# Optimization experiments

Measured on AMD Instinct MI355X. Metric: run time of the kernel, lower is better.

## Reference

```python
import jax, jax.numpy as jnp
import numpy as np

EPS_NORM = 1e-12
BN_EPS = 1e-5
TEMP = 0.07


def _l2norm(x, axis):
    n = jnp.sqrt(jnp.sum(x * x, axis=axis, keepdims=True))
    return x / jnp.maximum(n, EPS_NORM)


def _bn_eval(z, w, b):
    # inference-mode BatchNorm2d with running_mean=0, running_var=1
    s = w / jnp.sqrt(jnp.asarray(1.0 + BN_EPS, z.dtype))
    return z * s[None, :, None, None] + b[None, :, None, None]


def setup_inputs() -> dict:
    key = jax.random.key(0)
    ks = jax.random.split(key, 8)
    B, C, H, W = 16, 256, 64, 64
    KD, P = 128, 256
    x = jax.random.normal(ks[0], (B, C, H, W), jnp.float32)
    m_features = jax.random.normal(ks[1], (P, KD), jnp.float32)
    q_w = jax.random.normal(ks[2], (KD, C), jnp.float32) * 0.05
    k_w = jax.random.normal(ks[3], (KD, KD), jnp.float32) * 0.05
    v_w = jax.random.normal(ks[4], (KD, KD), jnp.float32) * 0.05
    o_w = jax.random.normal(ks[5], (C, KD), jnp.float32) * 0.05
    dw_w = jax.random.normal(ks[6], (C, 1, 3, 3), jnp.float32) * 0.1
    return {
        "x": x, "m_features": m_features,
        "q_w": q_w, "q_b": jnp.zeros((KD,), jnp.float32),
        "k_w": k_w, "k_b": jnp.zeros((KD,), jnp.float32),
        "v_w": v_w, "v_b": jnp.zeros((KD,), jnp.float32),
        "o_w": o_w, "o_b": jnp.zeros((C,), jnp.float32),
        "dw_w": dw_w,
        "bn1_w": jnp.ones((C,), jnp.float32), "bn1_b": jnp.zeros((C,), jnp.float32),
        "bn2_w": jnp.ones((C,), jnp.float32), "bn2_b": jnp.zeros((C,), jnp.float32),
        "gamma": jnp.ones((C,), jnp.float32) * 1e-5,
    }


def reference(x, m_features, q_w, q_b, k_w, k_b, v_w, v_b, o_w, o_b,
              dw_w, bn1_w, bn1_b, bn2_w, bn2_b, gamma):
    B, C, H, W = x.shape
    KD = q_w.shape[0]
    residual = x
    # q_proj 1x1 conv -> [B,KD,H,W], L2-normalize over channel dim
    q = jnp.einsum('bchw,kc->bkhw', x, q_w) + q_b[None, :, None, None]
    q = _l2norm(q, axis=1)
    q = q.reshape(B, KD, H * W).transpose(0, 2, 1)  # [B, HW, KD]
    # k/v projections of memory bank [P, KD]
    k = _l2norm(m_features @ k_w.T + k_b, axis=-1)
    v = m_features @ v_w.T + v_b
    # fp32 attention with clamped logits
    q32, k32, v32 = q.astype(jnp.float32), k.astype(jnp.float32), v.astype(jnp.float32)
    logits = jnp.clip(jnp.einsum('bnd,pd->bnp', q32, k32) / TEMP, -30.0, 30.0)
    attn = jax.nn.softmax(logits, axis=-1)
    out = jnp.einsum('bnp,pd->bnd', attn, v32).astype(x.dtype)
    out = out.transpose(0, 2, 1).reshape(B, KD, H, W)
    # out_proj 1x1 conv -> [B,C,H,W]
    out = jnp.einsum('bkhw,ck->bchw', out, o_w) + o_b[None, :, None, None]
    # local branch: depthwise 3x3 conv + BN + exact GELU
    local = jax.lax.conv_general_dilated(
        out, dw_w, window_strides=(1, 1), padding='SAME',
        feature_group_count=C,
        dimension_numbers=('NCHW', 'OIHW', 'NCHW'))
    local = jax.nn.gelu(_bn_eval(local, bn1_w, bn1_b), approximate=False)
    out = out + local
    return _bn_eval(residual + out * gamma[None, :, None, None], bn2_w, bn2_b)
```

## Files before the change

kernel.cpp:

```cpp
#include <hip/hip_runtime.h>
#include <hip/hip_bf16.h>
#include <math.h>

#define B_ 16
#define C_ 256
#define H_ 64
#define W_ 64
#define KD_ 128
#define P_ 256
#define HW_ (H_ * W_)

typedef __bf16 bf16;
typedef float f32x4_t __attribute__((ext_vector_type(4)));
typedef float f32x16_t __attribute__((ext_vector_type(16)));
typedef unsigned char u8;

__device__ __forceinline__ unsigned cvt_pk_fp8_lo(float a, float b, unsigned old) {
#if __has_builtin(__builtin_amdgcn_cvt_pk_fp8_f32)
    return __builtin_amdgcn_cvt_pk_fp8_f32(a, b, old, false);
#else
    unsigned r = old;
    asm("v_cvt_pk_fp8_f32 %0, %1, %2" : "+v"(r) : "v"(a), "v"(b));
    return r;
#endif
}
__device__ __forceinline__ unsigned cvt_pk_fp8_hi(float a, float b, unsigned old) {
#if __has_builtin(__builtin_amdgcn_cvt_pk_fp8_f32)
    return __builtin_amdgcn_cvt_pk_fp8_f32(a, b, old, true);
#else
    unsigned r = old;
    asm("v_cvt_pk_fp8_f32 %0, %1, %2 op_sel:[0,0,1]" : "+v"(r) : "v"(a), "v"(b));
    return r;
#endif
}
__device__ __forceinline__ uint2 pack8_fp8(const float* f) {
    uint2 r;
    r.x = cvt_pk_fp8_hi(f[2], f[3], cvt_pk_fp8_lo(f[0], f[1], 0u));
    r.y = cvt_pk_fp8_hi(f[6], f[7], cvt_pk_fp8_lo(f[4], f[5], 0u));
    return r;
}
template<int SEL>
__device__ __forceinline__ float fp8_to_f32(unsigned w) {
#if __has_builtin(__builtin_amdgcn_cvt_f32_fp8)
    return __builtin_amdgcn_cvt_f32_fp8(w, SEL);
#else
    float r;
    asm("v_cvt_f32_fp8 %0, %1" : "=v"(r) : "v"(w >> (SEL * 8)));
    return r;
#endif
}

__global__ __launch_bounds__(512, 8) void k_xpose(
    const float* __restrict__ x, u8* __restrict__ x8)
{
    __shared__ __align__(16) u8 tile[16 * 2048];
    const int cblk = blockIdx.x >> 1;
    const int ph   = blockIdx.x & 1;
    const int b    = blockIdx.y;
    const int t = threadIdx.x;

    {
        const int cl = t >> 5, sub = t & 31;
        const float* src = x + ((size_t)b * C_ + cblk * 16 + cl) * HW_ + ph * 2048;
#pragma unroll
        for (int i = 0; i < 16; ++i) {
            const f32x4_t v = *(const f32x4_t*)(src + (i * 32 + sub) * 4);
            const unsigned w = cvt_pk_fp8_hi(v[2], v[3],
                               cvt_pk_fp8_lo(v[0], v[1], 0u));
            *(unsigned*)&tile[cl * 2048 + (i * 32 + sub) * 4] = w;
        }
    }
    __syncthreads();
    {
        const int pr = t & 63;
        const int r0 = t >> 6;
#pragma unroll
        for (int it = 0; it < 4; ++it) {
            const int r = it * 8 + r0;
            const int lp = r * 64 + pr;
            union { u8 bytes[16]; uint4 u; } g;
#pragma unroll
            for (int c = 0; c < 16; ++c) g.bytes[c] = tile[c * 2048 + lp];
            const int h = ph * 32 + r;
            *(uint4*)(x8 + (((size_t)(b * 64 + h) * 16 + cblk) << 10) + pr * 16) = g.u;
        }
    }
}

__global__ __launch_bounds__(128) void k_prep1(
    const float* __restrict__ m_feat,
    const float* __restrict__ k_w, const float* __restrict__ k_b,
    const float* __restrict__ v_w, const float* __restrict__ v_b,
    float* __restrict__ kn_f, float* __restrict__ v_f)
{
    const int p = blockIdx.x;
    const int j = threadIdx.x;
    __shared__ float msh[KD_];
    __shared__ float red[2];
    msh[j] = m_feat[p * KD_ + j];
    __syncthreads();

    float ka = k_b[j];
    float va = v_b[j];
#pragma unroll 4
    for (int d = 0; d < KD_; ++d) {
        const float m = msh[d];
        ka = fmaf(m, k_w[j * KD_ + d], ka);
        va = fmaf(m, v_w[j * KD_ + d], va);
    }
    float s = ka * ka;
#pragma unroll
    for (int o = 1; o < 64; o <<= 1) s += __shfl_xor(s, o);
    if ((j & 63) == 0) red[j >> 6] = s;
    __syncthreads();
    s = red[0] + red[1];
    const float inv = 1.0f / (0.07f * fmaxf(sqrtf(s), 1e-12f));
    kn_f[p * KD_ + j] = ka * inv;
    v_f[p * KD_ + j] = va;
}

__global__ __launch_bounds__(256) void k_prep23(
    const float* __restrict__ o_w, const float* __restrict__ v_f,
    const float* __restrict__ q_w, const float* __restrict__ kn_f,
    u8* __restrict__ m28, u8* __restrict__ qw8, u8* __restrict__ kn8)
{
    if (blockIdx.x < 256) {
        const int c = blockIdx.x;
        const int p = threadIdx.x;
        __shared__ float osh[KD_];
        if (p < KD_) osh[p] = o_w[c * KD_ + p];
        __syncthreads();
        float acc = 0.f;
#pragma unroll 4
        for (int k = 0; k < KD_; ++k) acc = fmaf(osh[k], v_f[p * KD_ + k], acc);
        const int mt = c >> 5, r = c & 31;
        const int ks = p >> 4, sub = (p >> 3) & 1, jj = p & 7;
        const unsigned pk = cvt_pk_fp8_lo(acc * 16.0f, 0.f, 0u);
        m28[(((mt * 16 + ks) * 64) + sub * 32 + r) * 8 + jj] = (u8)(pk & 0xffu);
    } else {
        const int t = (blockIdx.x - 256) * 256 + threadIdx.x;
        float f[8];
        if (t < 4096) {
            const int lane = t & 63, g = t >> 6, mt = g >> 4, ks = g & 15;
            const int row = mt * 32 + (lane & 31), k0 = ks * 16 + (lane >> 5) * 8;
            const float* src = q_w + row * C_ + k0;
#pragma unroll
            for (int j = 0; j < 8; ++j) f[j] = src[j] * 16.0f;
            ((uint2*)qw8)[t] = pack8_fp8(f);
        } else {
            const int u = t - 4096;
            const int lane = u & 63, g = u >> 6, mt = g >> 3, ks = g & 7;
            const int row = mt * 32 + (lane & 31), k0 = ks * 16 + (lane >> 5) * 8;
            const float* src = kn_f + row * KD_ + k0;
#pragma unroll
            for (int j = 0; j < 8; ++j) f[j] = src[j];
            ((uint2*)kn8)[u] = pack8_fp8(f);
        }
    }
}

__global__ __launch_bounds__(512, 4) void k_attn(
    const u8* __restrict__ x8,
    const float* __restrict__ q_b, const float* __restrict__ o_b,
    const u8* __restrict__ qw8, const u8* __restrict__ kn8,
    const u8* __restrict__ m28, u8* __restrict__ outf8)
{
    __shared__ __align__(16) char lds[43008];
    char* const ebuf = lds;
    char* const qbuf = lds + 16384;
    float* const ss_lds   = (float*)(lds + 32768);
    float* const pmax_lds = (float*)(lds + 34816);
    float* const sum_lds  = (float*)(lds + 38912);

    const int rp = blockIdx.x;
    const int b = blockIdx.y;
    const int tid = threadIdx.x;
    const int lane = tid & 63;
    const int wid = tid >> 6;
    const int l31 = lane & 31;
    const int kh  = lane >> 5;

    const int mtA = wid & 3, nh = wid >> 2;
    {
        const u8* xrow = x8 + ((size_t)(b * 64 + rp * 2 + nh) << 14);
        f32x16_t qacc0, qacc1;
#pragma unroll
        for (int i = 0; i < 16; ++i) { qacc0[i] = 0.f; qacc1[i] = 0.f; }
#pragma unroll
        for (int ks = 0; ks < 16; ++ks) {
            const long a = *(const long*)(qw8 + ((mtA * 16 + ks) * 64 + lane) * 8);
            const long bx0 = *(const long*)(xrow + ks * 1024 + l31 * 16 + kh * 8);
            const long bx1 = *(const long*)(xrow + ks * 1024 + (32 + l31) * 16 + kh * 8);
            qacc0 = __builtin_amdgcn_mfma_f32_32x32x16_fp8_fp8(a, bx0, qacc0, 0, 0, 0);
            qacc1 = __builtin_amdgcn_mfma_f32_32x32x16_fp8_fp8(a, bx1, qacc1, 0, 0, 0);
        }
#pragma unroll
        for (int nt = 0; nt < 2; ++nt) {
            const int pix = nh * 64 + nt * 32 + l31;
            float ssp = 0.f;
#pragma unroll
            for (int g = 0; g < 4; ++g) {
                const f32x4_t qbv = *(const f32x4_t*)(q_b + mtA * 32 + g * 8 + kh * 4);
#pragma unroll
                for (int i = 0; i < 4; ++i) {
                    float qv = (nt == 0) ? qacc0[g * 4 + i] : qacc1[g * 4 + i];
                    qv += 16.0f * qbv[i];
                    if (nt == 0) qacc0[g * 4 + i] = qv; else qacc1[g * 4 + i] = qv;
                    ssp = fmaf(qv, qv, ssp);
                }
            }
            ssp += __shfl_xor(ssp, 32);
            if (lane < 32) ss_lds[pix * 4 + mtA] = ssp;
#pragma unroll
            for (int g = 0; g < 4; ++g) {
                const float e0 = (nt == 0) ? qacc0[g * 4 + 0] : qacc1[g * 4 + 0];
                const float e1 = (nt == 0) ? qacc0[g * 4 + 1] : qacc1[g * 4 + 1];
                const float e2 = (nt == 0) ? qacc0[g * 4 + 2] : qacc1[g * 4 + 2];
                const float e3 = (nt == 0) ? qacc0[g * 4 + 3] : qacc1[g * 4 + 3];
                const unsigned qw_ = cvt_pk_fp8_hi(e2, e3, cvt_pk_fp8_lo(e0, e1, 0u));
                *(unsigned*)(qbuf + pix * 128 +
                             ((mtA * 32 + g * 8 + kh * 4) ^ ((l31 & 15) << 3))) = qw_;
            }
        }
    }
    __syncthreads();

    f32x16_t lacc0, lacc1, lacc2, lacc3;
#pragma unroll
    for (int i = 0; i < 16; ++i) { lacc0[i] = 0.f; lacc1[i] = 0.f; lacc2[i] = 0.f; lacc3[i] = 0.f; }
#pragma unroll
    for (int ks = 0; ks < 8; ++ks) {
        const long a = *(const long*)(kn8 + ((wid * 8 + ks) * 64 + lane) * 8);
        const int ko = (ks * 16 + kh * 8) ^ ((l31 & 15) << 3);
        const long bq0 = *(const long*)(qbuf + (0 * 32 + l31) * 128 + ko);
        const long bq1 = *(const long*)(qbuf + (1 * 32 + l31) * 128 + ko);
        const long bq2 = *(const long*)(qbuf + (2 * 32 + l31) * 128 + ko);
        const long bq3 = *(const long*)(qbuf + (3 * 32 + l31) * 128 + ko);
        lacc0 = __builtin_amdgcn_mfma_f32_32x32x16_fp8_fp8(a, bq0, lacc0, 0, 0, 0);
        lacc1 = __builtin_amdgcn_mfma_f32_32x32x16_fp8_fp8(a, bq1, lacc1, 0, 0, 0);
        lacc2 = __builtin_amdgcn_mfma_f32_32x32x16_fp8_fp8(a, bq2, lacc2, 0, 0, 0);
        lacc3 = __builtin_amdgcn_mfma_f32_32x32x16_fp8_fp8(a, bq3, lacc3, 0, 0, 0);
    }
#pragma unroll
    for (int nt = 0; nt < 4; ++nt) {
        const int pix = nt * 32 + l31;
        float mx = -1e30f;
#pragma unroll
        for (int i = 0; i < 16; ++i) {
            const float lv = (nt == 0) ? lacc0[i] : (nt == 1) ? lacc1[i]
                           : (nt == 2) ? lacc2[i] : lacc3[i];
            mx = fmaxf(mx, lv);
        }
        mx = fmaxf(mx, __shfl_xor(mx, 32));
        if (lane < 32) pmax_lds[pix * 8 + wid] = mx;
    }
    __syncthreads();

#pragma unroll
    for (int nt = 0; nt < 4; ++nt) {
        const int pix = nt * 32 + l31;
        const f32x4_t s4 = *(const f32x4_t*)(ss_lds + pix * 4);
        const float qinv = 1.0f / fmaxf(sqrtf(s4[0] + s4[1] + s4[2] + s4[3]), 1e-12f);
        const f32x4_t ma = *(const f32x4_t*)(pmax_lds + pix * 8);
        const f32x4_t mb = *(const f32x4_t*)(pmax_lds + pix * 8 + 4);
        const float cof = 5.545177444479562f -
                          fmaxf(fmaxf(fmaxf(ma[0], ma[1]), fmaxf(ma[2], ma[3])),
                                fmaxf(fmaxf(mb[0], mb[1]), fmaxf(mb[2], mb[3]))) * qinv;
        float sm = 0.f;
#pragma unroll
        for (int g = 0; g < 4; ++g) {
            float e[4];
#pragma unroll
            for (int i = 0; i < 4; ++i) {
                const float lv = (nt == 0) ? lacc0[g * 4 + i] : (nt == 1) ? lacc1[g * 4 + i]
                               : (nt == 2) ? lacc2[g * 4 + i] : lacc3[g * 4 + i];
                e[i] = __expf(fmaf(lv, qinv, cof));
                sm += e[i];
            }
            const unsigned ew = cvt_pk_fp8_hi(e[2], e[3],
                                cvt_pk_fp8_lo(e[0], e[1], 0u));
            const int p0 = wid * 32 + g * 8 + kh * 4;
            *(unsigned*)(ebuf + pix * 256 + (p0 ^ (l31 << 3))) = ew;
        }
        sm += __shfl_xor(sm, 32);
        if (lane < 32) sum_lds[pix * 8 + wid] = sm;
    }
    __syncthreads();

    f32x16_t oacc0, oacc1, oacc2, oacc3;
#pragma unroll
    for (int i = 0; i < 16; ++i) { oacc0[i] = 0.f; oacc1[i] = 0.f; oacc2[i] = 0.f; oacc3[i] = 0.f; }
#pragma unroll
    for (int ks = 0; ks < 16; ++ks) {
        const long a = *(const long*)(m28 + ((wid * 16 + ks) * 64 + lane) * 8);
        const int ko = (ks * 16 + kh * 8);
        const long be0 = *(const long*)(ebuf + (0 * 32 + l31) * 256 + (ko ^ (l31 << 3)));
        const long be1 = *(const long*)(ebuf + (1 * 32 + l31) * 256 + (ko ^ (l31 << 3)));
        const long be2 = *(const long*)(ebuf + (2 * 32 + l31) * 256 + (ko ^ (l31 << 3)));
        const long be3 = *(const long*)(ebuf + (3 * 32 + l31) * 256 + (ko ^ (l31 << 3)));
        oacc0 = __builtin_amdgcn_mfma_f32_32x32x16_fp8_fp8(a, be0, oacc0, 0, 0, 0);
        oacc1 = __builtin_amdgcn_mfma_f32_32x32x16_fp8_fp8(a, be1, oacc1, 0, 0, 0);
        oacc2 = __builtin_amdgcn_mfma_f32_32x32x16_fp8_fp8(a, be2, oacc2, 0, 0, 0);
        oacc3 = __builtin_amdgcn_mfma_f32_32x32x16_fp8_fp8(a, be3, oacc3, 0, 0, 0);
    }
    {
        u8* const obase = outf8 + (size_t)b * C_ * HW_ + rp * 128;
        f32x4_t obv16[4];
#pragma unroll
        for (int g = 0; g < 4; ++g) {
            const f32x4_t t = *(const f32x4_t*)(o_b + wid * 32 + g * 8 + kh * 4);
            obv16[g] = t * 16.0f;
        }
#pragma unroll
        for (int nt = 0; nt < 4; ++nt) {
            const int p = nt * 32 + l31;
            const f32x4_t sa = *(const f32x4_t*)(sum_lds + p * 8);
            const f32x4_t sb = *(const f32x4_t*)(sum_lds + p * 8 + 4);
            const float rs16 = 1.0f / ((sa[0] + sa[1] + sa[2] + sa[3]) +
                                       (sb[0] + sb[1] + sb[2] + sb[3]));
            u8* const op = obase + p;
#pragma unroll
            for (int g = 0; g < 4; ++g) {
                float o[4];
#pragma unroll
                for (int i = 0; i < 4; ++i) {
                    const float av = (nt == 0) ? oacc0[g * 4 + i] : (nt == 1) ? oacc1[g * 4 + i]
                                   : (nt == 2) ? oacc2[g * 4 + i] : oacc3[g * 4 + i];
                    o[i] = fmaf(av, rs16, obv16[g][i]);
                }
                const unsigned u01 = cvt_pk_fp8_lo(o[0], o[1], 0u);
                const unsigned u23 = cvt_pk_fp8_lo(o[2], o[3], 0u);
                const int c = wid * 32 + g * 8 + kh * 4;
                op[(size_t)(c + 0) * HW_] = (u8)(u01 & 0xff);
                op[(size_t)(c + 1) * HW_] = (u8)((u01 >> 8) & 0xff);
                op[(size_t)(c + 2) * HW_] = (u8)(u23 & 0xff);
                op[(size_t)(c + 3) * HW_] = (u8)((u23 >> 8) & 0xff);
            }
        }
    }
}

__global__ __launch_bounds__(256, 4) void k_post(
    const float* __restrict__ x, const u8* __restrict__ outf8,
    const float* __restrict__ dw_w,
    const float* __restrict__ bn1_w, const float* __restrict__ bn1_b,
    const float* __restrict__ bn2_w, const float* __restrict__ bn2_b,
    const float* __restrict__ gamma, float* __restrict__ y)
{
    __shared__ __align__(16) u8 os8[64 + HW_ + 64];
    u8* const os = os8 + 64;
    const int bc = blockIdx.x;
    const int c = bc & (C_ - 1);
    const int tid = threadIdx.x;

    if (tid < 4)       *(uint4*)&os8[tid * 16] = make_uint4(0, 0, 0, 0);
    else if (tid < 8)  *(uint4*)&os8[64 + HW_ + (tid - 4) * 16] = make_uint4(0, 0, 0, 0);
    *(uint4*)&os[tid * 16] = *(const uint4*)(outf8 + (size_t)bc * HW_ + tid * 16);

    const float cbn = 0.99999500003750f;
    const float s1 = bn1_w[c] * cbn, b1 = bn1_b[c];
    const float s2 = bn2_w[c] * cbn, b2 = bn2_b[c];
    const float g = gamma[c];
    const float gc = g * 0.0625f;
    float kw[9];
#pragma unroll
    for (int j = 0; j < 9; ++j) kw[j] = dw_w[c * 9 + j] * 0.0625f;

    __syncthreads();

    const int q = tid & 15;
    const int c4 = q * 4;
    const int r0 = tid >> 4;
    const float* xc = x + (size_t)bc * HW_;
    float* yc = y + (size_t)bc * HW_;

#pragma unroll
    for (int k = 0; k < 4; ++k) {
        const int r = r0 + k * 16;
        const f32x4_t x4 = *(const f32x4_t*)(xc + r * 64 + c4);
        float vt[6], vm[6], vb[6];
        {
            const int rbt = r * 64, rbm = rbt + 64, rbb = rbt + 128;
            const unsigned uCt = *(const unsigned*)&os8[rbt + c4];
            const unsigned uCm = *(const unsigned*)&os8[rbm + c4];
            const unsigned uCb = *(const unsigned*)&os8[rbb + c4];
            vt[1] = fp8_to_f32<0>(uCt); vt[2] = fp8_to_f32<1>(uCt);
            vt[3] = fp8_to_f32<2>(uCt); vt[4] = fp8_to_f32<3>(uCt);
            vm[1] = fp8_to_f32<0>(uCm); vm[2] = fp8_to_f32<1>(uCm);
            vm[3] = fp8_to_f32<2>(uCm); vm[4] = fp8_to_f32<3>(uCm);
            vb[1] = fp8_to_f32<0>(uCb); vb[2] = fp8_to_f32<1>(uCb);
            vb[3] = fp8_to_f32<2>(uCb); vb[4] = fp8_to_f32<3>(uCb);
            if (q > 0) {
                vt[0] = fp8_to_f32<3>(*(const unsigned*)&os8[rbt + c4 - 4]);
                vm[0] = fp8_to_f32<3>(*(const unsigned*)&os8[rbm + c4 - 4]);
                vb[0] = fp8_to_f32<3>(*(const unsigned*)&os8[rbb + c4 - 4]);
            } else { vt[0] = vm[0] = vb[0] = 0.f; }
            if (q < 15) {
                vt[5] = fp8_to_f32<0>(*(const unsigned*)&os8[rbt + c4 + 4]);
                vm[5] = fp8_to_f32<0>(*(const unsigned*)&os8[rbm + c4 + 4]);
                vb[5] = fp8_to_f32<0>(*(const unsigned*)&os8[rbb + c4 + 4]);
            } else { vt[5] = vm[5] = vb[5] = 0.f; }
        }
        f32x4_t y4;
#pragma unroll
        for (int j = 0; j < 4; ++j) {
            float conv = kw[0] * vt[j];
            conv = fmaf(kw[1], vt[j + 1], conv);
            conv = fmaf(kw[2], vt[j + 2], conv);
            conv = fmaf(kw[3], vm[j], conv);
            conv = fmaf(kw[4], vm[j + 1], conv);
            conv = fmaf(kw[5], vm[j + 2], conv);
            conv = fmaf(kw[6], vb[j], conv);
            conv = fmaf(kw[7], vb[j + 1], conv);
            conv = fmaf(kw[8], vb[j + 2], conv);
            const float t = fmaf(conv, s1, b1);
            const float lg = t / (1.0f + __expf(-1.702f * t));
            y4[j] = fmaf(lg, g, fmaf(vm[j + 1], gc, x4[j])) * s2 + b2;
        }
        *(f32x4_t*)(yc + r * 64 + c4) = y4;
    }
}

extern "C" void kernel_launch(void* const* d_in, const int* in_sizes, int n_in,
                              void* d_out, int out_size, void* d_ws, size_t ws_size,
                              hipStream_t stream)
{
    const float* x     = (const float*)d_in[0];
    const float* m_f   = (const float*)d_in[1];
    const float* q_w   = (const float*)d_in[2];
    const float* q_b   = (const float*)d_in[3];
    const float* k_w   = (const float*)d_in[4];
    const float* k_b   = (const float*)d_in[5];
    const float* v_w   = (const float*)d_in[6];
    const float* v_b   = (const float*)d_in[7];
    const float* o_w   = (const float*)d_in[8];
    const float* o_b   = (const float*)d_in[9];
    const float* dw_w  = (const float*)d_in[10];
    const float* bn1_w = (const float*)d_in[11];
    const float* bn1_b = (const float*)d_in[12];
    const float* bn2_w = (const float*)d_in[13];
    const float* bn2_b = (const float*)d_in[14];
    const float* gamma = (const float*)d_in[15];

    char* ws = (char*)d_ws;
    u8*    qw8   = (u8*)(ws);
    u8*    kn8   = (u8*)(ws + (32 << 10));
    u8*    m28   = (u8*)(ws + (64 << 10));
    u8*    x8    = (u8*)(ws + (1 << 20));
    u8*    outf8 = (u8*)(ws + (17 << 20));
    float* kn_f  = (float*)(ws + (34 << 20));
    float* v_f   = (float*)(ws + (34 << 20) + (128 << 10));

    k_xpose<<<dim3(32, B_), dim3(512), 0, stream>>>(x, x8);
    k_prep1<<<dim3(P_), dim3(128), 0, stream>>>(m_f, k_w, k_b, v_w, v_b,
                                                kn_f, v_f);
    k_prep23<<<dim3(288), dim3(256), 0, stream>>>(o_w, v_f, q_w, kn_f,
                                                  m28, qw8, kn8);
    k_attn<<<dim3(H_ / 2, B_), dim3(512), 0, stream>>>(x8, q_b, o_b, qw8, kn8,
                                                       m28, outf8);
    k_post<<<dim3(B_ * C_), dim3(256), 0, stream>>>(
        x, outf8, dw_w, bn1_w, bn1_b, bn2_w, bn2_b, gamma, (float*)d_out);
}
```

Measured before the change: 81.25 us.

## Merge transpose and k/v prep kernels, hoist kn8 loads, nontemporal post stores

Fuses the x transpose/fp8 cast kernel and the k/v projection kernel into one launch, with extra blocks each handling four memory rows. This removes one kernel launch and lets the small prep work overlap the bandwidth-bound transpose. In the attention kernel, the kn8 fragments are loaded into registers up front so their latency overlaps the q projection. k_post gets a higher launch-bounds occupancy hint and writes its output with nontemporal stores, which may raise register pressure or change cache behaviour.

```diff
diff --git a/kernel.cpp b/kernel.cpp
--- a/kernel.cpp
+++ b/kernel.cpp
@@ -49,74 +49,84 @@
     return r;
 #endif
 }
-
-__global__ __launch_bounds__(512, 8) void k_xpose(
-    const float* __restrict__ x, u8* __restrict__ x8)
-{
-    __shared__ __align__(16) u8 tile[16 * 2048];
-    const int cblk = blockIdx.x >> 1;
-    const int ph   = blockIdx.x & 1;
-    const int b    = blockIdx.y;
-    const int t = threadIdx.x;
-
-    {
-        const int cl = t >> 5, sub = t & 31;
-        const float* src = x + ((size_t)b * C_ + cblk * 16 + cl) * HW_ + ph * 2048;
-#pragma unroll
-        for (int i = 0; i < 16; ++i) {
-            const f32x4_t v = *(const f32x4_t*)(src + (i * 32 + sub) * 4);
-            const unsigned w = cvt_pk_fp8_hi(v[2], v[3],
-                               cvt_pk_fp8_lo(v[0], v[1], 0u));
-            *(unsigned*)&tile[cl * 2048 + (i * 32 + sub) * 4] = w;
-        }
-    }
-    __syncthreads();
-    {
-        const int pr = t & 63;
-        const int r0 = t >> 6;
-#pragma unroll
-        for (int it = 0; it < 4; ++it) {
-            const int r = it * 8 + r0;
-            const int lp = r * 64 + pr;
-            union { u8 bytes[16]; uint4 u; } g;
-#pragma unroll
-            for (int c = 0; c < 16; ++c) g.bytes[c] = tile[c * 2048 + lp];
-            const int h = ph * 32 + r;
-            *(uint4*)(x8 + (((size_t)(b * 64 + h) * 16 + cblk) << 10) + pr * 16) = g.u;
-        }
-    }
-}
-
-__global__ __launch_bounds__(128) void k_prep1(
+template<typename T>
+__device__ __forceinline__ void nt_store(T* p, T v) {
+#if __has_builtin(__builtin_nontemporal_store)
+    __builtin_nontemporal_store(v, p);
+#else
+    *p = v;
+#endif
+}
+
+__global__ __launch_bounds__(512, 8) void k_pre_a(
+    const float* __restrict__ x, u8* __restrict__ x8,
     const float* __restrict__ m_feat,
     const float* __restrict__ k_w, const float* __restrict__ k_b,
     const float* __restrict__ v_w, const float* __restrict__ v_b,
     float* __restrict__ kn_f, float* __restrict__ v_f)
 {
-    const int p = blockIdx.x;
-    const int j = threadIdx.x;
-    __shared__ float msh[KD_];
-    __shared__ float red[2];
-    msh[j] = m_feat[p * KD_ + j];
-    __syncthreads();
-
-    float ka = k_b[j];
-    float va = v_b[j];
+    __shared__ __align__(16) u8 tile[16 * 2048];
+    __shared__ float msh4[4][KD_];
+    __shared__ float red4[4][2];
+    const int u = blockIdx.x;
+    const int t = threadIdx.x;
+
+    if (u < 512) {
+        const int b    = u >> 5;
+        const int v_   = u & 31;
+        const int cblk = v_ >> 1;
+        const int ph   = v_ & 1;
+        {
+            const int cl = t >> 5, sub = t & 31;
+            const float* src = x + ((size_t)b * C_ + cblk * 16 + cl) * HW_ + ph * 2048;
+#pragma unroll
+            for (int i = 0; i < 16; ++i) {
+                const f32x4_t v = *(const f32x4_t*)(src + (i * 32 + sub) * 4);
+                const unsigned w = cvt_pk_fp8_hi(v[2], v[3],
+                                   cvt_pk_fp8_lo(v[0], v[1], 0u));
+                *(unsigned*)&tile[cl * 2048 + (i * 32 + sub) * 4] = w;
+            }
+        }
+        __syncthreads();
+        {
+            const int pr = t & 63;
+            const int r0 = t >> 6;
+#pragma unroll
+            for (int it = 0; it < 4; ++it) {
+                const int r = it * 8 + r0;
+                const int lp = r * 64 + pr;
+                union { u8 bytes[16]; uint4 uu; } g;
+#pragma unroll
+                for (int c = 0; c < 16; ++c) g.bytes[c] = tile[c * 2048 + lp];
+                const int h = ph * 32 + r;
+                *(uint4*)(x8 + (((size_t)(b * 64 + h) * 16 + cblk) << 10) + pr * 16) = g.uu;
+            }
+        }
+    } else {
+        const int sub = t >> 7;
+        const int j   = t & 127;
+        const int p   = (u - 512) * 4 + sub;
+        msh4[sub][j] = m_feat[p * KD_ + j];
+        __syncthreads();
+
+        float ka = k_b[j];
+        float va = v_b[j];
 #pragma unroll 4
-    for (int d = 0; d < KD_; ++d) {
-        const float m = msh[d];
-        ka = fmaf(m, k_w[j * KD_ + d], ka);
-        va = fmaf(m, v_w[j * KD_ + d], va);
-    }
-    float s = ka * ka;
-#pragma unroll
-    for (int o = 1; o < 64; o <<= 1) s += __shfl_xor(s, o);
-    if ((j & 63) == 0) red[j >> 6] = s;
-    __syncthreads();
-    s = red[0] + red[1];
-    const float inv = 1.0f / (0.07f * fmaxf(sqrtf(s), 1e-12f));
-    kn_f[p * KD_ + j] = ka * inv;
-    v_f[p * KD_ + j] = va;
+        for (int d = 0; d < KD_; ++d) {
+            const float m = msh4[sub][d];
+            ka = fmaf(m, k_w[j * KD_ + d], ka);
+            va = fmaf(m, v_w[j * KD_ + d], va);
+        }
+        float s = ka * ka;
+#pragma unroll
+        for (int o = 1; o < 64; o <<= 1) s += __shfl_xor(s, o);
+        if ((j & 63) == 0) red4[sub][j >> 6] = s;
+        __syncthreads();
+        s = red4[sub][0] + red4[sub][1];
+        const float inv = 1.0f / (0.07f * fmaxf(sqrtf(s), 1e-12f));
+        kn_f[p * KD_ + j] = ka * inv;
+        v_f[p * KD_ + j] = va;
+    }
 }
 
 __global__ __launch_bounds__(256) void k_prep23(
@@ -180,6 +190,11 @@
     const int l31 = lane & 31;
     const int kh  = lane >> 5;
 
+    long kna[8];
+#pragma unroll
+    for (int ks = 0; ks < 8; ++ks)
+        kna[ks] = *(const long*)(kn8 + ((wid * 8 + ks) * 64 + lane) * 8);
+
     const int mtA = wid & 3, nh = wid >> 2;
     {
         const u8* xrow = x8 + ((size_t)(b * 64 + rp * 2 + nh) << 14);
@@ -230,16 +245,15 @@
     for (int i = 0; i < 16; ++i) { lacc0[i] = 0.f; lacc1[i] = 0.f; lacc2[i] = 0.f; lacc3[i] = 0.f; }
 #pragma unroll
     for (int ks = 0; ks < 8; ++ks) {
-        const long a = *(const long*)(kn8 + ((wid * 8 + ks) * 64 + lane) * 8);
         const int ko = (ks * 16 + kh * 8) ^ ((l31 & 15) << 3);
         const long bq0 = *(const long*)(qbuf + (0 * 32 + l31) * 128 + ko);
         const long bq1 = *(const long*)(qbuf + (1 * 32 + l31) * 128 + ko);
         const long bq2 = *(const long*)(qbuf + (2 * 32 + l31) * 128 + ko);
         const long bq3 = *(const long*)(qbuf + (3 * 32 + l31) * 128 + ko);
-        lacc0 = __builtin_amdgcn_mfma_f32_32x32x16_fp8_fp8(a, bq0, lacc0, 0, 0, 0);
-        lacc1 = __builtin_amdgcn_mfma_f32_32x32x16_fp8_fp8(a, bq1, lacc1, 0, 0, 0);
-        lacc2 = __builtin_amdgcn_mfma_f32_32x32x16_fp8_fp8(a, bq2, lacc2, 0, 0, 0);
-        lacc3 = __builtin_amdgcn_mfma_f32_32x32x16_fp8_fp8(a, bq3, lacc3, 0, 0, 0);
+        lacc0 = __builtin_amdgcn_mfma_f32_32x32x16_fp8_fp8(kna[ks], bq0, lacc0, 0, 0, 0);
+        lacc1 = __builtin_amdgcn_mfma_f32_32x32x16_fp8_fp8(kna[ks], bq1, lacc1, 0, 0, 0);
+        lacc2 = __builtin_amdgcn_mfma_f32_32x32x16_fp8_fp8(kna[ks], bq2, lacc2, 0, 0, 0);
+        lacc3 = __builtin_amdgcn_mfma_f32_32x32x16_fp8_fp8(kna[ks], bq3, lacc3, 0, 0, 0);
     }
 #pragma unroll
     for (int nt = 0; nt < 4; ++nt) {
@@ -340,7 +354,7 @@
     }
 }
 
-__global__ __launch_bounds__(256, 4) void k_post(
+__global__ __launch_bounds__(256, 8) void k_post(
     const float* __restrict__ x, const u8* __restrict__ outf8,
     const float* __restrict__ dw_w,
     const float* __restrict__ bn1_w, const float* __restrict__ bn1_b,
@@ -417,7 +431,7 @@
             const float lg = t / (1.0f + __expf(-1.702f * t));
             y4[j] = fmaf(lg, g, fmaf(vm[j + 1], gc, x4[j])) * s2 + b2;
         }
-        *(f32x4_t*)(yc + r * 64 + c4) = y4;
+        nt_store((f32x4_t*)(yc + r * 64 + c4), y4);
     }
 }
 
@@ -451,9 +465,8 @@
     float* kn_f  = (float*)(ws + (34 << 20));
     float* v_f   = (float*)(ws + (34 << 20) + (128 << 10));
 
-    k_xpose<<<dim3(32, B_), dim3(512), 0, stream>>>(x, x8);
-    k_prep1<<<dim3(P_), dim3(128), 0, stream>>>(m_f, k_w, k_b, v_w, v_b,
-                                                kn_f, v_f);
+    k_pre_a<<<dim3(576), dim3(512), 0, stream>>>(x, x8, m_f, k_w, k_b, v_w, v_b,
+                                                 kn_f, v_f);
     k_prep23<<<dim3(288), dim3(256), 0, stream>>>(o_w, v_f, q_w, kn_f,
                                                   m28, qw8, kn8);
     k_attn<<<dim3(H_ / 2, B_), dim3(512), 0, stream>>>(x8, q_b, o_b, qw8, kn8,
```

Result: slower. 86.52 us (+6.5%).
